# Kernel tuning notes

Hardware: AMD Instinct MI355X
Metric: run time of the kernel (lower is better)

Reference implementation:

```python
import jax, jax.numpy as jnp
import numpy as np

L, H, D, N, M, P, C, IMG, B = 12, 12, 768, 197, 3072, 16, 3, 224, 16
SKIP_AT = (3, 6, 9, 12)


def pos_emb(n, d):
    i = jnp.arange(n, dtype=jnp.float32)[:, None]
    j = jnp.arange(d)[None, :]
    je = (j // 2) * 2  # j for even, j-1 for odd
    ang = i / jnp.power(10000.0, je.astype(jnp.float32) / d)
    return jnp.where(j % 2 == 0, jnp.sin(ang), jnp.cos(ang))  # [n, d]


def layer_norm(x, g, b):
    mu = x.mean(-1, keepdims=True)
    var = x.var(-1, keepdims=True)
    return (x - mu) / jnp.sqrt(var + 1e-5) * g + b


def setup_inputs() -> dict:
    key = jax.random.key(0)
    ks = jax.random.split(key, 16)
    s = 0.02
    f32 = jnp.float32
    return {
        "images": jax.random.normal(ks[0], (B, C, IMG, IMG), f32),
        "class_token": jax.random.uniform(ks[1], (1, D), f32),
        "Wp": jax.random.normal(ks[2], (D, P * P * C), f32) * s,
        "bp": jnp.zeros((D,), f32),
        "Wq": jax.random.normal(ks[3], (L, H, D, D), f32) * s,
        "bq": jnp.zeros((L, H, D), f32),
        "Wk": jax.random.normal(ks[4], (L, H, D, D), f32) * s,
        "bk": jnp.zeros((L, H, D), f32),
        "Wv": jax.random.normal(ks[5], (L, H, D, D), f32) * s,
        "bv": jnp.zeros((L, H, D), f32),
        "Wm": jax.random.normal(ks[6], (L, N, H * N), f32) * s,
        "bm": jnp.zeros((L, N), f32),
        "g1": jnp.ones((L, D), f32),
        "be1": jnp.zeros((L, D), f32),
        "W1": jax.random.normal(ks[7], (L, M, D), f32) * s,
        "b1": jnp.zeros((L, M), f32),
        "W2": jax.random.normal(ks[8], (L, D, M), f32) * s,
        "b2": jnp.zeros((L, D), f32),
        "g2": jnp.ones((L, D), f32),
        "be2": jnp.zeros((L, D), f32),
    }


def reference(images, class_token, Wp, bp, Wq, bq, Wk, bk, Wv, bv, Wm, bm,
              g1, be1, W1, b1, W2, b2, g2, be2):
    b = images.shape[0]
    Hn, Wn = IMG // P, IMG // P
    # einops 'b c (patch_x h) (patch_y w) -> b (h w) (patch_x patch_y c)'
    x = images.reshape(b, C, P, Hn, P, Wn).transpose(0, 3, 5, 2, 4, 1)
    patches = x.reshape(b, Hn * Wn, P * P * C)
    tokens = patches @ Wp.T + bp  # [b, N-1, D]
    cls = jnp.broadcast_to(class_token[None], (b, 1, D))
    out = jnp.concatenate([cls, tokens], axis=1) + pos_emb(N, D)[None]
    scale = 1.0 / jnp.sqrt(jnp.float32(N - 1))
    skips = []
    for l in range(L):
        x0 = out
        q = jnp.einsum('bnd,hed->bhne', x0, Wq[l]) + bq[l][None, :, None, :]
        k = jnp.einsum('bnd,hed->bhne', x0, Wk[l]) + bk[l][None, :, None, :]
        v = jnp.einsum('bnd,hed->bhne', x0, Wv[l]) + bv[l][None, :, None, :]
        attn = jax.nn.softmax(jnp.einsum('bhne,bhme->bhnm', q, k) * scale, axis=-1)
        o = jnp.einsum('bhnm,bhme->bhne', attn, v).reshape(b, H * N, D)
        # transpose -> [b, D, H*N], Linear(H*N -> N), transpose back
        msa = jnp.einsum('bfd,nf->bnd', o, Wm[l]) + bm[l][None, :, None]
        x1 = layer_norm(x0 + msa, g1[l], be1[l])
        hdn = jax.nn.gelu(x1 @ W1[l].T + b1[l], approximate=False)
        out = layer_norm(x1 + (hdn @ W2[l].T + b2[l]), g2[l], be2[l])
        if l + 1 in SKIP_AT:
            skips.append(out[:, 1:, :])
    return (out[:, 1:, :], *skips)
```

## Files before the change

### kernel.cpp

```cpp
#include <hip/hip_runtime.h>
#include <cstdint>
#include <cstddef>

typedef __bf16 bf16;
typedef __bf16 bf16x8 __attribute__((ext_vector_type(8)));
typedef float f32x4 __attribute__((ext_vector_type(4)));

#define DEVINL __device__ __forceinline__

typedef const __attribute__((address_space(1))) void* as1cv;
typedef __attribute__((address_space(3))) void* as3v;

DEVINL void gload16(const bf16* g, bf16* l) {
    __builtin_amdgcn_global_load_lds((as1cv)g, (as3v)l, 16, 0, 0);
}

static constexpr int Lh = 12, Hh = 12, Dh = 768, Nh = 197, Mh = 3072, Bh = 16;
static constexpr int BN   = Bh * Nh;
static constexpr int NPAT = Bh * 196;
static constexpr int HD   = Hh * Dh;
static constexpr int QKN  = 2 * HD;
static constexpr int NP   = 256;
static constexpr int FHN  = Hh * Nh;
static constexpr int FP   = 2368;
static constexpr size_t SEC = (size_t)Bh * 196 * Dh;
static constexpr long LSqk = (long)QKN * Dh;
static constexpr long PART = (long)BN * Dh;

template<int AF32, int BF32, int OUTBF, int BIAS, int ACT, int ZFILL>
__global__ __launch_bounds__(256, 3) void gemm_bt(
    const void* __restrict__ Av, long sAy, long sAz, int lda,
    const void* __restrict__ Bv, long sBy, long sBz, int ldb,
    void* __restrict__ Cv, long sCy, long sCz, int ldc,
    const float* __restrict__ bias, long sBiasY,
    int Mv, int Nv, int K, int tilesN, int kChunk)
{
    __shared__ __align__(16) bf16 Asm[128 * 32];
    __shared__ __align__(16) bf16 Bsm[128 * 32];
    const int bx = blockIdx.x;
    const int tm = bx / tilesN, tn = bx % tilesN;
    const long aoff = (long)blockIdx.y * sAy + (long)blockIdx.z * sAz + (long)tm * 128 * lda;
    const long boff = (long)blockIdx.y * sBy + (long)blockIdx.z * sBz + (long)tn * 128 * ldb;
    const int tid = threadIdx.x;
    const int lane = tid & 63, wid = tid >> 6;
    const int ar = tid >> 2, ac = (tid & 3) << 3;
    const bf16* Ag = (const bf16*)Av + aoff + (long)ar * lda + ac;
    const bf16* Bg = (const bf16*)Bv + boff + (long)ar * ldb + ac;
    const float* Af = (const float*)Av + aoff + (long)ar * lda + ac;
    const float* Bf = (const float*)Bv + boff + (long)ar * ldb + ac;
    bf16* lA = Asm + wid * 512;
    bf16* lB = Bsm + wid * 512;
    const int mw = (wid >> 1) * 64, nw = (wid & 1) * 64;
    const int fr = lane & 15, fq = lane >> 4;
    const int kBeg = kChunk ? blockIdx.y * kChunk : 0;
    const int kEnd = kChunk ? min(K, kBeg + kChunk) : K;
    f32x4 acc[4][4] = {};
    for (int k0 = kBeg; k0 < kEnd; k0 += 32) {
        if (AF32) {
            const float* p0 = Af + k0;
            const float* p1 = p0 + (long)64 * lda;
            f32x4 a0 = *(const f32x4*)p0, a1 = *(const f32x4*)(p0 + 4);
            f32x4 a2 = *(const f32x4*)p1, a3 = *(const f32x4*)(p1 + 4);
            bf16x8 r0, r1;
#pragma unroll
            for (int i = 0; i < 4; i++) { r0[i] = (bf16)a0[i]; r0[i + 4] = (bf16)a1[i];
                                          r1[i] = (bf16)a2[i]; r1[i + 4] = (bf16)a3[i]; }
            *(bf16x8*)&Asm[ar * 32 + ac] = r0;
            *(bf16x8*)&Asm[(ar + 64) * 32 + ac] = r1;
        } else {
            gload16(Ag + k0, lA);
            gload16(Ag + (long)64 * lda + k0, lA + 2048);
        }
        if (BF32) {
            const float* p0 = Bf + k0;
            const float* p1 = p0 + (long)64 * ldb;
            f32x4 a0 = *(const f32x4*)p0, a1 = *(const f32x4*)(p0 + 4);
            f32x4 a2 = *(const f32x4*)p1, a3 = *(const f32x4*)(p1 + 4);
            bf16x8 r0, r1;
#pragma unroll
            for (int i = 0; i < 4; i++) { r0[i] = (bf16)a0[i]; r0[i + 4] = (bf16)a1[i];
                                          r1[i] = (bf16)a2[i]; r1[i + 4] = (bf16)a3[i]; }
            *(bf16x8*)&Bsm[ar * 32 + ac] = r0;
            *(bf16x8*)&Bsm[(ar + 64) * 32 + ac] = r1;
        } else {
            gload16(Bg + k0, lB);
            gload16(Bg + (long)64 * ldb + k0, lB + 2048);
        }
        __syncthreads();
        bf16x8 af[4], bv[4];
#pragma unroll
        for (int i = 0; i < 4; i++) af[i] = *(const bf16x8*)&Asm[(mw + i * 16 + fr) * 32 + (fq << 3)];
#pragma unroll
        for (int j = 0; j < 4; j++) bv[j] = *(const bf16x8*)&Bsm[(nw + j * 16 + fr) * 32 + (fq << 3)];
#pragma unroll
        for (int i = 0; i < 4; i++)
#pragma unroll
            for (int j = 0; j < 4; j++)
                acc[i][j] = __builtin_amdgcn_mfma_f32_16x16x32_bf16(af[i], bv[j], acc[i][j], 0, 0, 0);
        __syncthreads();
    }
    const long cb = (long)blockIdx.y * sCy + (long)blockIdx.z * sCz;
    const float* biasp = bias ? bias + (long)blockIdx.y * sBiasY : nullptr;
#pragma unroll
    for (int i = 0; i < 4; i++) {
        const int row0 = tm * 128 + mw + i * 16 + fq * 4;
#pragma unroll
        for (int j = 0; j < 4; j++) {
            const int col = tn * 128 + nw + j * 16 + fr;
            const bool cok = (col < Nv);
            if (!cok && !ZFILL) continue;
            float bc = (BIAS == 1 && cok) ? biasp[col] : 0.f;
#pragma unroll
            for (int r = 0; r < 4; r++) {
                const int rr = row0 + r;
                if (rr >= Mv) continue;
                float v;
                if (cok) {
                    v = acc[i][j][r];
                    if (BIAS == 1) v += bc;
                    if (BIAS == 2) v += biasp[rr];
                    if (ACT) v = 0.5f * v * (1.f + erff(v * 0.70710678118654752f));
                } else v = 0.f;
                const long ci = cb + (long)rr * ldc + col;
                if (OUTBF) ((bf16*)Cv)[ci] = (bf16)v;
                else       ((float*)Cv)[ci] = v;
            }
        }
    }
}

__global__ __launch_bounds__(512, 2) void qksoft_k(
    const bf16* __restrict__ qkb, bf16* __restrict__ P)
{
    __shared__ __align__(16) bf16 Qs[128 * 32];
    __shared__ __align__(16) bf16 Ks[256 * 32];
    __shared__ float redM[2][64][4];
    __shared__ float redS[2][64][4];
    const int rt = blockIdx.x, h = blockIdx.y, b = blockIdx.z;
    const int tid = threadIdx.x;
    const int lane = tid & 63, wid = tid >> 6;
    const int wr = wid >> 2, wc = wid & 3;
    const int fr = lane & 15, fq = lane >> 4;
    const int ar = tid >> 2, ac = (tid & 3) << 3;
    const bf16* Qg = qkb + ((size_t)b * Nh + rt * 128 + ar) * QKN + h * Dh + ac;
    const bf16* Kg = qkb + ((size_t)b * Nh + ar) * QKN + HD + h * Dh + ac;
    bf16* lQ = Qs + wid * 512;
    bf16* lK = Ks + wid * 512;
    f32x4 acc[4][4] = {};
    for (int k0 = 0; k0 < 768; k0 += 32) {
        gload16(Qg + k0, lQ);
        gload16(Kg + k0, lK);
        gload16(Kg + (size_t)128 * QKN + k0, lK + 4096);
        __syncthreads();
        bf16x8 af[4], bv[4];
#pragma unroll
        for (int i = 0; i < 4; i++) af[i] = *(const bf16x8*)&Qs[(wr * 64 + i * 16 + fr) * 32 + (fq << 3)];
#pragma unroll
        for (int j = 0; j < 4; j++) bv[j] = *(const bf16x8*)&Ks[(wc * 64 + j * 16 + fr) * 32 + (fq << 3)];
#pragma unroll
        for (int i = 0; i < 4; i++)
#pragma unroll
            for (int j = 0; j < 4; j++)
                acc[i][j] = __builtin_amdgcn_mfma_f32_16x16x32_bf16(af[i], bv[j], acc[i][j], 0, 0, 0);
        __syncthreads();
    }
    const float scale = 1.f / 14.f;
    float mx[4][4];
#pragma unroll
    for (int i = 0; i < 4; i++)
#pragma unroll
        for (int r = 0; r < 4; r++) {
            float m0 = -3e30f;
#pragma unroll
            for (int j = 0; j < 4; j++) {
                const int m = wc * 64 + j * 16 + fr;
                float v = (m < Nh) ? acc[i][j][r] * scale : -3e30f;
                acc[i][j][r] = v;
                m0 = fmaxf(m0, v);
            }
            m0 = fmaxf(m0, __shfl_xor(m0, 1));
            m0 = fmaxf(m0, __shfl_xor(m0, 2));
            m0 = fmaxf(m0, __shfl_xor(m0, 4));
            m0 = fmaxf(m0, __shfl_xor(m0, 8));
            mx[i][r] = m0;
        }
    if (fr == 0) {
#pragma unroll
        for (int i = 0; i < 4; i++)
#pragma unroll
            for (int r = 0; r < 4; r++) redM[wr][i * 16 + fq * 4 + r][wc] = mx[i][r];
    }
    __syncthreads();
    float sm[4][4];
#pragma unroll
    for (int i = 0; i < 4; i++)
#pragma unroll
        for (int r = 0; r < 4; r++) {
            const int row = i * 16 + fq * 4 + r;
            const float rm = fmaxf(fmaxf(redM[wr][row][0], redM[wr][row][1]),
                                   fmaxf(redM[wr][row][2], redM[wr][row][3]));
            float s0 = 0.f;
#pragma unroll
            for (int j = 0; j < 4; j++) {
                const float e = expf(acc[i][j][r] - rm);
                acc[i][j][r] = e;
                s0 += e;
            }
            s0 += __shfl_xor(s0, 1);
            s0 += __shfl_xor(s0, 2);
            s0 += __shfl_xor(s0, 4);
            s0 += __shfl_xor(s0, 8);
            sm[i][r] = s0;
        }
    if (fr == 0) {
#pragma unroll
        for (int i = 0; i < 4; i++)
#pragma unroll
            for (int r = 0; r < 4; r++) redS[wr][i * 16 + fq * 4 + r][wc] = sm[i][r];
    }
    __syncthreads();
    bf16* Pb = P + ((size_t)(b * Hh + h) * NP + rt * 128) * NP;
#pragma unroll
    for (int i = 0; i < 4; i++)
#pragma unroll
        for (int r = 0; r < 4; r++) {
            const int row = i * 16 + fq * 4 + r;
            const float s = redS[wr][row][0] + redS[wr][row][1] + redS[wr][row][2] + redS[wr][row][3];
            const float inv = 1.f / s;
#pragma unroll
            for (int j = 0; j < 4; j++)
                Pb[(size_t)(wr * 64 + row) * NP + wc * 64 + j * 16 + fr] = (bf16)(acc[i][j][r] * inv);
        }
}

__global__ __launch_bounds__(256) void cvt_k(const float* __restrict__ in, bf16* __restrict__ out, long n) {
    const long i = ((long)blockIdx.x * 256 + threadIdx.x) * 8;
    if (i >= n) return;
    f32x4 a = *(const f32x4*)(in + i);
    f32x4 b = *(const f32x4*)(in + i + 4);
    bf16x8 r;
#pragma unroll
    for (int j = 0; j < 4; j++) { r[j] = (bf16)a[j]; r[j + 4] = (bf16)b[j]; }
    *(bf16x8*)(out + i) = r;
}

__global__ __launch_bounds__(256) void cvt_s_k(const float* __restrict__ in, bf16* __restrict__ out,
                                               long perLayer, long dstStride, long dstOff, long total) {
    const long i = ((long)blockIdx.x * 256 + threadIdx.x) * 8;
    if (i >= total) return;
    const long l = i / perLayer, r = i % perLayer;
    f32x4 a = *(const f32x4*)(in + i);
    f32x4 b = *(const f32x4*)(in + i + 4);
    bf16x8 v;
#pragma unroll
    for (int j = 0; j < 4; j++) { v[j] = (bf16)a[j]; v[j + 4] = (bf16)b[j]; }
    *(bf16x8*)(out + l * dstStride + dstOff + r) = v;
}

__global__ void qkbias_k(const float* __restrict__ bq, const float* __restrict__ bk, float* __restrict__ dst) {
    const int idx = blockIdx.x * 256 + threadIdx.x;
    if (idx >= Lh * QKN) return;
    const int l = idx / QKN, c = idx % QKN;
    dst[idx] = (c < HD) ? bq[l * HD + c] : bk[l * HD + c - HD];
}

__global__ void patch_k(const float* __restrict__ images, bf16* __restrict__ patches) {
    const long idx = (long)blockIdx.x * 256 + threadIdx.x;
    if (idx >= (long)NPAT * Dh) return;
    const int r = (int)(idx / Dh), f = (int)(idx % Dh);
    const int b = r / 196, pi = r % 196, h = pi / 14, w = pi % 14;
    const int px = f / 48, rem = f % 48, py = rem / 3, c = rem % 3;
    patches[idx] = (bf16)images[(((long)(b * 3 + c) * 224) + px * 14 + h) * 224 + py * 14 + w];
}

__global__ void assemble_k(const float* __restrict__ tokens, const float* __restrict__ cls,
                           float* __restrict__ x, bf16* __restrict__ xbf) {
    const long idx = (long)blockIdx.x * 256 + threadIdx.x;
    if (idx >= (long)BN * Dh) return;
    const int r = (int)(idx / Dh), d = (int)(idx % Dh);
    const int b = r / Nh, n = r % Nh;
    const int je = d & ~1;
    const float ang = (float)n / powf(10000.f, (float)je / 768.f);
    const float pe = (d & 1) ? cosf(ang) : sinf(ang);
    const float val = (n == 0) ? (cls[d] + pe)
                               : (tokens[((long)b * 196 + (n - 1)) * Dh + d] + pe);
    x[idx] = val;
    xbf[idx] = (bf16)val;
}

__global__ void wmpad_k(const float* __restrict__ Wm, bf16* __restrict__ WmP) {
    const long idx = (long)blockIdx.x * 256 + threadIdx.x;
    if (idx >= (long)Lh * 256 * FP) return;
    const int l = (int)(idx / (256 * FP));
    const int rem = (int)(idx % (256 * FP));
    const int n = rem / FP, f = rem % FP;
    bf16 v = (bf16)0.f;
    if (n < Nh && f < FHN) v = (bf16)Wm[((long)l * Nh + n) * FHN + f];
    WmP[idx] = v;
}

__global__ void otpad_k(bf16* __restrict__ oT, int cb) {
    const int idx = blockIdx.x * 256 + threadIdx.x;
    if (idx >= cb * Dh * 4) return;
    const int b = idx / (Dh * 4), rem = idx % (Dh * 4), e = rem / 4, f = rem % 4;
    oT[((long)b * Dh + e) * FP + FHN + f] = (bf16)0.f;
}

__global__ __launch_bounds__(256) void softmax_k(const float* __restrict__ S, bf16* __restrict__ P) {
    const int tid = threadIdx.x, lane = tid & 63, wv = tid >> 6;
    const long rr = (long)blockIdx.x * 4 + wv;
    const int bh = (int)(rr / Nh), n = (int)(rr % Nh);
    const float* s = S + ((long)bh * Nh + n) * NP;
    bf16* p = P + ((long)bh * NP + n) * NP;
    float v[4]; float mx = -1e30f;
#pragma unroll
    for (int i = 0; i < 4; i++) {
        const int c = lane + i * 64;
        const float t = (c < Nh) ? s[c] * (1.f / 14.f) : -1e30f;
        v[i] = t; mx = fmaxf(mx, t);
    }
    for (int o = 32; o; o >>= 1) mx = fmaxf(mx, __shfl_xor(mx, o));
    float sum = 0.f;
#pragma unroll
    for (int i = 0; i < 4; i++) {
        const int c = lane + i * 64;
        v[i] = (c < Nh) ? expf(v[i] - mx) : 0.f;
        sum += v[i];
    }
    for (int o = 32; o; o >>= 1) sum += __shfl_xor(sum, o);
    const float inv = 1.f / sum;
#pragma unroll
    for (int i = 0; i < 4; i++) p[lane + i * 64] = (bf16)(v[i] * inv);
}

template<int BIAS_ROW, int NPART>
__global__ __launch_bounds__(256) void add_ln_k(
    const float* __restrict__ in1, const float* __restrict__ in2, long pstride,
    const float* __restrict__ bias, const float* __restrict__ gamma, const float* __restrict__ beta,
    float* __restrict__ outF, bf16* __restrict__ outBF,
    float* __restrict__ dst0, float* __restrict__ dst1)
{
    const int r = blockIdx.x;
    const int b = r / Nh, n = r % Nh;
    const long base = (long)r * Dh;
    const int tid = threadIdx.x;
    const float rowb = BIAS_ROW ? bias[n] : 0.f;
    float v[3]; float s = 0.f, s2 = 0.f;
#pragma unroll
    for (int i = 0; i < 3; i++) {
        const int d = tid + 256 * i;
        float t = in1[base + d] + (BIAS_ROW ? rowb : bias[d]);
#pragma unroll
        for (int pp = 0; pp < NPART; pp++) t += in2[pp * pstride + base + d];
        v[i] = t; s += t; s2 += t * t;
    }
    for (int o = 32; o; o >>= 1) { s += __shfl_xor(s, o); s2 += __shfl_xor(s2, o); }
    __shared__ float red[8];
    const int lane = tid & 63, wv = tid >> 6;
    if (lane == 0) { red[wv] = s; red[4 + wv] = s2; }
    __syncthreads();
    s  = red[0] + red[1] + red[2] + red[3];
    s2 = red[4] + red[5] + red[6] + red[7];
    const float mu = s * (1.f / 768.f);
    const float var = s2 * (1.f / 768.f) - mu * mu;
    const float rs = rsqrtf(var + 1e-5f);
    const long ob = ((long)b * 196 + (n - 1)) * Dh;
#pragma unroll
    for (int i = 0; i < 3; i++) {
        const int d = tid + 256 * i;
        const float y = (v[i] - mu) * rs * gamma[d] + beta[d];
        outF[base + d] = y;
        outBF[base + d] = (bf16)y;
        if (n > 0) {
            if (dst0) dst0[ob + d] = y;
            if (dst1) dst1[ob + d] = y;
        }
    }
}

static inline size_t al256(size_t x) { return (x + 255) & ~(size_t)255; }

extern "C" void kernel_launch(void* const* d_in, const int* in_sizes, int n_in,
                              void* d_out, int out_size, void* d_ws, size_t ws_size,
                              hipStream_t stream) {
    (void)in_sizes; (void)n_in; (void)out_size;
    const float* images = (const float*)d_in[0];
    const float* cls    = (const float*)d_in[1];
    const float* Wp     = (const float*)d_in[2];
    const float* bp     = (const float*)d_in[3];
    const float* Wq     = (const float*)d_in[4];
    const float* bq     = (const float*)d_in[5];
    const float* Wk     = (const float*)d_in[6];
    const float* bk     = (const float*)d_in[7];
    const float* Wv     = (const float*)d_in[8];
    const float* bv     = (const float*)d_in[9];
    const float* Wm     = (const float*)d_in[10];
    const float* bm     = (const float*)d_in[11];
    const float* g1     = (const float*)d_in[12];
    const float* be1    = (const float*)d_in[13];
    const float* W1     = (const float*)d_in[14];
    const float* b1     = (const float*)d_in[15];
    const float* W2     = (const float*)d_in[16];
    const float* b2     = (const float*)d_in[17];
    const float* g2     = (const float*)d_in[18];
    const float* be2    = (const float*)d_in[19];
    float* out = (float*)d_out;

    const size_t xB    = al256(3152ull * 768 * 4);
    const size_t xbfB  = al256(3328ull * 768 * 2);
    const size_t x1B   = al256(3152ull * 768 * 4);
    const size_t x1bfB = al256(3200ull * 768 * 2);
    const size_t msaB  = al256(4ull * PART * 4);
    const size_t mlp2B = al256(4ull * PART * 4);
    const size_t wmpB  = al256(12ull * 256 * FP * 2);
    const size_t qkbB  = al256((size_t)Lh * QKN * 4);
    const size_t persistB = xB + xbfB + x1B + x1bfB + msaB + mlp2B + wmpB + qkbB;
    const size_t hdnB  = al256(3200ull * 3072 * 2);
    const size_t preB  = al256(3200ull * 768 * 2) + al256(3136ull * 768 * 4);
    const size_t wqkvB = al256((size_t)Lh * HD * Dh * 2);
    const size_t w12B  = al256((size_t)Lh * Mh * Dh * 2);
    const size_t wpB   = al256(768ull * 768 * 2);
    const size_t weightsB = 3 * wqkvB + 2 * w12B + wpB;

    auto chunk_bytes = [&](int cb, size_t& qbB_o, size_t& vtB_o, size_t& sB_o) -> size_t {
        const size_t qbRows = (size_t)((cb * 197 + 127) / 128 + 1) * 128;
        size_t qbB = al256(qbRows * HD * 2);
        size_t vtB = al256((size_t)cb * Hh * Dh * NP * 2);
        size_t sB  = al256((size_t)cb * Hh * Nh * NP * 4);
        size_t c = 2 * qbB + vtB + sB;
        if (c < hdnB) c = hdnB;
        if (c < preB) c = preB;
        qbB_o = qbB; vtB_o = vtB; sB_o = sB;
        return c;
    };
    const size_t margin = (size_t)(8u << 20);
    const size_t pBf  = al256((size_t)Bh * Hh * NP * NP * 2);
    const size_t otBf = al256((size_t)Bh * Dh * FP * 2);
    size_t qbBf, vtBf, sBf;
    size_t chunkF = chunk_bytes(16, qbBf, vtBf, sBf) + pBf + otBf;
    bool fused = (chunkF + persistB + weightsB + margin <= ws_size);

    int CB = 16; bool useCvt = true;
    size_t qbB, vtB, sB, chunkB;
    if (fused) {
        chunkB = chunkF; qbB = qbBf; vtB = vtBf; sB = sBf;
    } else {
        for (;;) {
            chunkB = chunk_bytes(CB, qbB, vtB, sB);
            if (chunkB + persistB + weightsB + margin <= ws_size) break;
            if (CB == 1) { useCvt = false; break; }
            CB >>= 1;
        }
        if (!useCvt) {
            CB = 16;
            for (;;) {
                chunkB = chunk_bytes(CB, qbB, vtB, sB);
                if (chunkB + persistB + margin <= ws_size || CB == 1) break;
                CB >>= 1;
            }
        }
    }

    char* wsb = (char*)d_ws;
    bf16*  qb  = (bf16*)wsb;
    bf16*  kb  = (bf16*)(wsb + qbB);
    bf16*  vT  = (bf16*)(wsb + 2 * qbB);
    float* S   = (float*)(wsb + 2 * qbB + vtB);
    bf16*  P2  = (bf16*)(wsb + 2 * qbB + vtB + sB);
    bf16*  oT2 = (bf16*)(wsb + 2 * qbB + vtB + sB + pBf);
    bf16*  oT  = fused ? oT2 : qb;
    bf16*  P   = fused ? P2  : kb;
    bf16*  hdn = (bf16*)wsb;
    bf16*  patches = (bf16*)wsb;
    float* tokens  = (float*)(wsb + al256(3200ull * 768 * 2));
    char* p = wsb + chunkB;
    float* x    = (float*)p; p += xB;
    bf16*  xbf  = (bf16*) p; p += xbfB;
    float* x1   = (float*)p; p += x1B;
    bf16*  x1bf = (bf16*) p; p += x1bfB;
    float* msaP = (float*)p; p += msaB;
    float* mlp2P= (float*)p; p += mlp2B;
    bf16*  WmP  = (bf16*) p; p += wmpB;
    float* qkbiasF = (float*)p; p += qkbB;
    bf16 *WqkB = nullptr, *WvB = nullptr, *W1B = nullptr, *W2B = nullptr, *WpB = nullptr;
    const bool cvt = fused || useCvt;
    if (cvt) {
        WqkB = (bf16*)p; p += 2 * wqkvB;
        WvB  = (bf16*)p; p += wqkvB;
        W1B  = (bf16*)p; p += w12B;
        W2B  = (bf16*)p; p += w12B;
        WpB  = (bf16*)p; p += wpB;
    }

    if (cvt) {
        const long nqkv = (long)Lh * HD * Dh;
        const long n12  = (long)Lh * Mh * Dh;
        const int gq = (int)((nqkv / 8 + 255) / 256);
        const int g12 = (int)((n12 / 8 + 255) / 256);
        cvt_s_k<<<gq, 256, 0, stream>>>(Wq, WqkB, (long)HD * Dh, LSqk, 0, nqkv);
        cvt_s_k<<<gq, 256, 0, stream>>>(Wk, WqkB, (long)HD * Dh, LSqk, (long)HD * Dh, nqkv);
        cvt_k<<<gq, 256, 0, stream>>>(Wv, WvB, nqkv);
        cvt_k<<<g12, 256, 0, stream>>>(W1, W1B, n12);
        cvt_k<<<g12, 256, 0, stream>>>(W2, W2B, n12);
        cvt_k<<<(768 * 768 / 8 + 255) / 256, 256, 0, stream>>>(Wp, WpB, 768 * 768);
        qkbias_k<<<(Lh * QKN + 255) / 256, 256, 0, stream>>>(bq, bk, qkbiasF);
    }

    patch_k<<<9408, 256, 0, stream>>>(images, patches);
    if (cvt)
        gemm_bt<0, 0, 0, 1, 0, 0><<<dim3(25 * 6), 256, 0, stream>>>(
            patches, 0, 0, 768, WpB, 0, 0, 768, tokens, 0, 0, 768, bp, 0, NPAT, 768, 768, 6, 0);
    else
        gemm_bt<0, 1, 0, 1, 0, 0><<<dim3(25 * 6), 256, 0, stream>>>(
            patches, 0, 0, 768, Wp, 0, 0, 768, tokens, 0, 0, 768, bp, 0, NPAT, 768, 768, 6, 0);
    assemble_k<<<9456, 256, 0, stream>>>(tokens, cls, x, xbf);
    wmpad_k<<<28416, 256, 0, stream>>>(Wm, WmP);
    if (fused) otpad_k<<<16 * 12, 256, 0, stream>>>(oT2, 16);

    const int NCH = 16 / CB;
    const int tilesQ = (CB * 197 + 127) / 128;

    for (int l = 0; l < 12; l++) {
        const float* Wq_l = Wq + (size_t)l * HD * Dh;
        const float* Wk_l = Wk + (size_t)l * HD * Dh;
        const float* Wv_l = Wv + (size_t)l * HD * Dh;
        const bf16* WqkB_l = cvt ? WqkB + (size_t)l * LSqk : nullptr;
        const bf16* WqB_l = WqkB_l;
        const bf16* WkB_l = cvt ? WqkB_l + (size_t)HD * Dh : nullptr;
        const bf16* WvB_l = cvt ? WvB + (size_t)l * HD * Dh : nullptr;
        const float* bq_l = bq + (size_t)l * HD;
        const float* bk_l = bk + (size_t)l * HD;
        const float* bv_l = bv + (size_t)l * HD;
        const bf16*  WmP_l = WmP + (size_t)l * 256 * FP;
        const float* bm_l = bm + (size_t)l * Nh;
        const float* g1_l = g1 + (size_t)l * Dh;  const float* be1_l = be1 + (size_t)l * Dh;
        const float* W1_l = W1 + (size_t)l * Mh * Dh; const float* b1_l = b1 + (size_t)l * Mh;
        const float* W2_l = W2 + (size_t)l * Dh * Mh; const float* b2_l = b2 + (size_t)l * Dh;
        const bf16* W1B_l = cvt ? W1B + (size_t)l * Mh * Dh : nullptr;
        const bf16* W2B_l = cvt ? W2B + (size_t)l * Mh * Dh : nullptr;
        const float* g2_l = g2 + (size_t)l * Dh;  const float* be2_l = be2 + (size_t)l * Dh;

        if (fused) {
            gemm_bt<0, 0, 1, 1, 0, 0><<<dim3(25 * 144), 256, 0, stream>>>(
                xbf, 0, 0, 768, WqkB_l, 0, 0, 768, qb, 0, 0, QKN,
                qkbiasF + (size_t)l * QKN, 0, BN, QKN, 768, 144, 0);
            gemm_bt<0, 0, 1, 2, 0, 1><<<dim3(12, 12, 16), 256, 0, stream>>>(
                WvB_l, (long)Dh * Dh, 0, 768,
                xbf, 0, (long)Nh * Dh, 768,
                vT, (long)Dh * NP, (long)Hh * Dh * NP, NP,
                bv_l, Dh, 768, Nh, 768, 2, 0);
            qksoft_k<<<dim3(2, Hh, Bh), 512, 0, stream>>>(qb, P);
            gemm_bt<0, 0, 1, 0, 0, 0><<<dim3(12, 12, 16), 256, 0, stream>>>(
                vT, (long)Dh * NP, (long)Hh * Dh * NP, NP,
                P, (long)NP * NP, (long)Hh * NP * NP, NP,
                oT, (long)Nh, (long)Dh * FP, FP,
                nullptr, 0, Dh, Nh, NP, 2, 0);
            gemm_bt<0, 0, 0, 0, 0, 0><<<dim3(12, 4, 16), 256, 0, stream>>>(
                WmP_l, 0, 0, FP,
                oT, 0, (long)Dh * FP, FP,
                msaP, PART, (long)Nh * Dh, Dh,
                nullptr, 0, Nh, Dh, FP, 6, 608);
        } else {
            for (int c = 0; c < NCH; c++) {
                const size_t r0 = (size_t)c * CB * Nh;
                if (useCvt) {
                    gemm_bt<0, 0, 1, 1, 0, 0><<<dim3(tilesQ * 72), 256, 0, stream>>>(
                        xbf + r0 * Dh, 0, 0, 768, WqB_l, 0, 0, 768, qb, 0, 0, HD, bq_l, 0, CB * Nh, HD, 768, 72, 0);
                    gemm_bt<0, 0, 1, 1, 0, 0><<<dim3(tilesQ * 72), 256, 0, stream>>>(
                        xbf + r0 * Dh, 0, 0, 768, WkB_l, 0, 0, 768, kb, 0, 0, HD, bk_l, 0, CB * Nh, HD, 768, 72, 0);
                    gemm_bt<0, 0, 1, 2, 0, 1><<<dim3(12, 12, CB), 256, 0, stream>>>(
                        WvB_l, (long)Dh * Dh, 0, 768,
                        xbf + r0 * Dh, 0, (long)Nh * Dh, 768,
                        vT, (long)Dh * NP, (long)Hh * Dh * NP, NP,
                        bv_l, Dh, 768, Nh, 768, 2, 0);
                } else {
                    gemm_bt<0, 1, 1, 1, 0, 0><<<dim3(tilesQ * 72), 256, 0, stream>>>(
                        xbf + r0 * Dh, 0, 0, 768, Wq_l, 0, 0, 768, qb, 0, 0, HD, bq_l, 0, CB * Nh, HD, 768, 72, 0);
                    gemm_bt<0, 1, 1, 1, 0, 0><<<dim3(tilesQ * 72), 256, 0, stream>>>(
                        xbf + r0 * Dh, 0, 0, 768, Wk_l, 0, 0, 768, kb, 0, 0, HD, bk_l, 0, CB * Nh, HD, 768, 72, 0);
                    gemm_bt<1, 0, 1, 2, 0, 1><<<dim3(12, 12, CB), 256, 0, stream>>>(
                        Wv_l, (long)Dh * Dh, 0, 768,
                        xbf + r0 * Dh, 0, (long)Nh * Dh, 768,
                        vT, (long)Dh * NP, (long)Hh * Dh * NP, NP,
                        bv_l, Dh, 768, Nh, 768, 2, 0);
                }
                gemm_bt<0, 0, 0, 0, 0, 0><<<dim3(4, 12, CB), 256, 0, stream>>>(
                    qb, Dh, (long)Nh * HD, HD,
                    kb, Dh, (long)Nh * HD, HD,
                    S, (long)Nh * NP, (long)Hh * Nh * NP, NP,
                    nullptr, 0, Nh, Nh, 768, 2, 0);
                softmax_k<<<CB * 591, 256, 0, stream>>>(S, P);
                otpad_k<<<CB * 12, 256, 0, stream>>>(oT, CB);
                gemm_bt<0, 0, 1, 0, 0, 0><<<dim3(12, 12, CB), 256, 0, stream>>>(
                    vT, (long)Dh * NP, (long)Hh * Dh * NP, NP,
                    P, (long)NP * NP, (long)Hh * NP * NP, NP,
                    oT, (long)Nh, (long)Dh * FP, FP,
                    nullptr, 0, Dh, Nh, NP, 2, 0);
                gemm_bt<0, 0, 0, 0, 0, 0><<<dim3(12, 4, CB), 256, 0, stream>>>(
                    WmP_l, 0, 0, FP,
                    oT, 0, (long)Dh * FP, FP,
                    msaP + r0 * Dh, PART, (long)Nh * Dh, Dh,
                    nullptr, 0, Nh, Dh, FP, 6, 608);
            }
        }
        add_ln_k<1, 4><<<BN, 256, 0, stream>>>(x, msaP, PART, bm_l, g1_l, be1_l, x1, x1bf, nullptr, nullptr);
        if (cvt) {
            gemm_bt<0, 0, 1, 1, 1, 0><<<dim3(25 * 24), 256, 0, stream>>>(
                x1bf, 0, 0, 768, W1B_l, 0, 0, 768, hdn, 0, 0, Mh, b1_l, 0, BN, Mh, 768, 24, 0);
            gemm_bt<0, 0, 0, 0, 0, 0><<<dim3(25 * 6, 4, 1), 256, 0, stream>>>(
                hdn, 0, 0, Mh, W2B_l, 0, 0, Mh, mlp2P, PART, 0, Dh, nullptr, 0, BN, Dh, Mh, 6, 768);
        } else {
            gemm_bt<0, 1, 1, 1, 1, 0><<<dim3(25 * 24), 256, 0, stream>>>(
                x1bf, 0, 0, 768, W1_l, 0, 0, 768, hdn, 0, 0, Mh, b1_l, 0, BN, Mh, 768, 24, 0);
            gemm_bt<0, 1, 0, 0, 0, 0><<<dim3(25 * 6, 4, 1), 256, 0, stream>>>(
                hdn, 0, 0, Mh, W2_l, 0, 0, Mh, mlp2P, PART, 0, Dh, nullptr, 0, BN, Dh, Mh, 6, 768);
        }
        float* d0 = nullptr; float* d1 = nullptr;
        if (l == 2)  d0 = out + 1 * SEC;
        if (l == 5)  d0 = out + 2 * SEC;
        if (l == 8)  d0 = out + 3 * SEC;
        if (l == 11) { d0 = out; d1 = out + 4 * SEC; }
        add_ln_k<0, 4><<<BN, 256, 0, stream>>>(x1, mlp2P, PART, b2_l, g2_l, be2_l, x, xbf, d0, d1);
    }
}
```

Baseline: 6.228 ms.

## Fuse V projection into single QKV GEMM and transpose V separately

Concatenates the bf16 Q, K and V weights and their biases so that one GEMM produces Q, K and V in a single row-major buffer. The separate batched, zero-filled V-transposed GEMM is replaced by a small LDS tile-transpose kernel that writes V into the padded vT layout. The fused GEMM gets a larger grid and better occupancy, and X is read once instead of twice, in exchange for an extra transpose pass over V and a larger intermediate buffer. The workspace sizing for the fused path is recomputed to match.

```diff
diff --git a/kernel.cpp b/kernel.cpp
--- a/kernel.cpp
+++ b/kernel.cpp
@@ -20,11 +20,12 @@
 static constexpr int NPAT = Bh * 196;
 static constexpr int HD   = Hh * Dh;
 static constexpr int QKN  = 2 * HD;
+static constexpr int QKV3 = 3 * HD;
 static constexpr int NP   = 256;
 static constexpr int FHN  = Hh * Nh;
 static constexpr int FP   = 2368;
 static constexpr size_t SEC = (size_t)Bh * 196 * Dh;
-static constexpr long LSqk = (long)QKN * Dh;
+static constexpr long LS3 = (long)QKV3 * Dh;
 static constexpr long PART = (long)BN * Dh;
 
 template<int AF32, int BF32, int OUTBF, int BIAS, int ACT, int ZFILL>
@@ -142,15 +143,15 @@
     const int wr = wid >> 2, wc = wid & 3;
     const int fr = lane & 15, fq = lane >> 4;
     const int ar = tid >> 2, ac = (tid & 3) << 3;
-    const bf16* Qg = qkb + ((size_t)b * Nh + rt * 128 + ar) * QKN + h * Dh + ac;
-    const bf16* Kg = qkb + ((size_t)b * Nh + ar) * QKN + HD + h * Dh + ac;
+    const bf16* Qg = qkb + ((size_t)b * Nh + rt * 128 + ar) * QKV3 + h * Dh + ac;
+    const bf16* Kg = qkb + ((size_t)b * Nh + ar) * QKV3 + HD + h * Dh + ac;
     bf16* lQ = Qs + wid * 512;
     bf16* lK = Ks + wid * 512;
     f32x4 acc[4][4] = {};
     for (int k0 = 0; k0 < 768; k0 += 32) {
         gload16(Qg + k0, lQ);
         gload16(Kg + k0, lK);
-        gload16(Kg + (size_t)128 * QKN + k0, lK + 4096);
+        gload16(Kg + (size_t)128 * QKV3 + k0, lK + 4096);
         __syncthreads();
         bf16x8 af[4], bv[4];
 #pragma unroll
@@ -233,6 +234,31 @@
         }
 }
 
+__global__ __launch_bounds__(256) void vtrans_k(const bf16* __restrict__ qkv, bf16* __restrict__ vT) {
+    __shared__ bf16 t[64][72];
+    const int eb = (blockIdx.x >> 2) << 6;
+    const int nb = (blockIdx.x & 3) << 6;
+    const int h = blockIdx.y, b = blockIdx.z;
+    const int tid = threadIdx.x;
+    const int lr = tid >> 2;
+    const int lc = (tid & 3) << 4;
+    const int n = nb + lr;
+    if (n < Nh) {
+        const bf16* src = qkv + (size_t)(b * Nh + n) * QKV3 + 2 * HD + h * Dh + eb + lc;
+        *(bf16x8*)&t[lr][lc] = *(const bf16x8*)src;
+        *(bf16x8*)&t[lr][lc + 8] = *(const bf16x8*)(src + 8);
+    } else {
+        bf16x8 z = {};
+        *(bf16x8*)&t[lr][lc] = z; *(bf16x8*)&t[lr][lc + 8] = z;
+    }
+    __syncthreads();
+    bf16* dst = vT + ((size_t)(b * Hh + h) * Dh + eb + lr) * NP + nb + lc;
+    bf16x8 o0, o1;
+#pragma unroll
+    for (int j = 0; j < 8; j++) { o0[j] = t[lc + j][lr]; o1[j] = t[lc + 8 + j][lr]; }
+    *(bf16x8*)dst = o0; *(bf16x8*)(dst + 8) = o1;
+}
+
 __global__ __launch_bounds__(256) void cvt_k(const float* __restrict__ in, bf16* __restrict__ out, long n) {
     const long i = ((long)blockIdx.x * 256 + threadIdx.x) * 8;
     if (i >= n) return;
@@ -257,11 +283,16 @@
     *(bf16x8*)(out + l * dstStride + dstOff + r) = v;
 }
 
-__global__ void qkbias_k(const float* __restrict__ bq, const float* __restrict__ bk, float* __restrict__ dst) {
+__global__ void qkvbias_k(const float* __restrict__ bq, const float* __restrict__ bk,
+                          const float* __restrict__ bv, float* __restrict__ dst) {
     const int idx = blockIdx.x * 256 + threadIdx.x;
-    if (idx >= Lh * QKN) return;
-    const int l = idx / QKN, c = idx % QKN;
-    dst[idx] = (c < HD) ? bq[l * HD + c] : bk[l * HD + c - HD];
+    if (idx >= Lh * QKV3) return;
+    const int l = idx / QKV3, c = idx % QKV3;
+    float v;
+    if (c < HD) v = bq[l * HD + c];
+    else if (c < 2 * HD) v = bk[l * HD + c - HD];
+    else v = bv[l * HD + c - 2 * HD];
+    dst[idx] = v;
 }
 
 __global__ void patch_k(const float* __restrict__ images, bf16* __restrict__ patches) {
@@ -413,14 +444,24 @@
     const size_t msaB  = al256(4ull * PART * 4);
     const size_t mlp2B = al256(4ull * PART * 4);
     const size_t wmpB  = al256(12ull * 256 * FP * 2);
-    const size_t qkbB  = al256((size_t)Lh * QKN * 4);
-    const size_t persistB = xB + xbfB + x1B + x1bfB + msaB + mlp2B + wmpB + qkbB;
+    const size_t biasB = al256((size_t)Lh * QKV3 * 4);
+    const size_t persistB = xB + xbfB + x1B + x1bfB + msaB + mlp2B + wmpB + biasB;
     const size_t hdnB  = al256(3200ull * 3072 * 2);
     const size_t preB  = al256(3200ull * 768 * 2) + al256(3136ull * 768 * 4);
     const size_t wqkvB = al256((size_t)Lh * HD * Dh * 2);
     const size_t w12B  = al256((size_t)Lh * Mh * Dh * 2);
     const size_t wpB   = al256(768ull * 768 * 2);
     const size_t weightsB = 3 * wqkvB + 2 * w12B + wpB;
+
+    const size_t qkvbB = al256(3328ull * QKV3 * 2);
+    const size_t vtBf  = al256((size_t)Bh * Hh * Dh * NP * 2);
+    const size_t pBf   = al256((size_t)Bh * Hh * NP * NP * 2);
+    const size_t otBf  = al256((size_t)Bh * Dh * FP * 2);
+    size_t chunkF = qkvbB + vtBf + pBf + otBf;
+    if (chunkF < hdnB) chunkF = hdnB;
+    if (chunkF < preB) chunkF = preB;
+    const size_t margin = (size_t)(8u << 20);
+    const bool fused = (chunkF + persistB + weightsB + margin <= ws_size);
 
     auto chunk_bytes = [&](int cb, size_t& qbB_o, size_t& vtB_o, size_t& sB_o) -> size_t {
         const size_t qbRows = (size_t)((cb * 197 + 127) / 128 + 1) * 128;
@@ -433,17 +474,10 @@
         qbB_o = qbB; vtB_o = vtB; sB_o = sB;
         return c;
     };
-    const size_t margin = (size_t)(8u << 20);
-    const size_t pBf  = al256((size_t)Bh * Hh * NP * NP * 2);
-    const size_t otBf = al256((size_t)Bh * Dh * FP * 2);
-    size_t qbBf, vtBf, sBf;
-    size_t chunkF = chunk_bytes(16, qbBf, vtBf, sBf) + pBf + otBf;
-    bool fused = (chunkF + persistB + weightsB + margin <= ws_size);
-
     int CB = 16; bool useCvt = true;
     size_t qbB, vtB, sB, chunkB;
     if (fused) {
-        chunkB = chunkF; qbB = qbBf; vtB = vtBf; sB = sBf;
+        chunkB = chunkF; qbB = vtB = sB = 0;
     } else {
         for (;;) {
             chunkB = chunk_bytes(CB, qbB, vtB, sB);
@@ -462,12 +496,15 @@
     }
 
     char* wsb = (char*)d_ws;
+    bf16*  qkvb = (bf16*)wsb;
+    bf16*  vT2  = (bf16*)(wsb + qkvbB);
+    bf16*  P2   = (bf16*)(wsb + qkvbB + vtBf);
+    bf16*  oT2  = (bf16*)(wsb + qkvbB + vtBf + pBf);
     bf16*  qb  = (bf16*)wsb;
     bf16*  kb  = (bf16*)(wsb + qbB);
-    bf16*  vT  = (bf16*)(wsb + 2 * qbB);
+    bf16*  vTf = (bf16*)(wsb + 2 * qbB);
     float* S   = (float*)(wsb + 2 * qbB + vtB);
-    bf16*  P2  = (bf16*)(wsb + 2 * qbB + vtB + sB);
-    bf16*  oT2 = (bf16*)(wsb + 2 * qbB + vtB + sB + pBf);
+    bf16*  vT  = fused ? vT2 : vTf;
     bf16*  oT  = fused ? oT2 : qb;
     bf16*  P   = fused ? P2  : kb;
     bf16*  hdn = (bf16*)wsb;
@@ -481,12 +518,11 @@
     float* msaP = (float*)p; p += msaB;
     float* mlp2P= (float*)p; p += mlp2B;
     bf16*  WmP  = (bf16*) p; p += wmpB;
-    float* qkbiasF = (float*)p; p += qkbB;
-    bf16 *WqkB = nullptr, *WvB = nullptr, *W1B = nullptr, *W2B = nullptr, *WpB = nullptr;
+    float* qkvbias = (float*)p; p += biasB;
+    bf16 *WqkvB = nullptr, *W1B = nullptr, *W2B = nullptr, *WpB = nullptr;
     const bool cvt = fused || useCvt;
     if (cvt) {
-        WqkB = (bf16*)p; p += 2 * wqkvB;
-        WvB  = (bf16*)p; p += wqkvB;
+        WqkvB = (bf16*)p; p += 3 * wqkvB;
         W1B  = (bf16*)p; p += w12B;
         W2B  = (bf16*)p; p += w12B;
         WpB  = (bf16*)p; p += wpB;
@@ -497,13 +533,13 @@
         const long n12  = (long)Lh * Mh * Dh;
         const int gq = (int)((nqkv / 8 + 255) / 256);
         const int g12 = (int)((n12 / 8 + 255) / 256);
-        cvt_s_k<<<gq, 256, 0, stream>>>(Wq, WqkB, (long)HD * Dh, LSqk, 0, nqkv);
-        cvt_s_k<<<gq, 256, 0, stream>>>(Wk, WqkB, (long)HD * Dh, LSqk, (long)HD * Dh, nqkv);
-        cvt_k<<<gq, 256, 0, stream>>>(Wv, WvB, nqkv);
+        cvt_s_k<<<gq, 256, 0, stream>>>(Wq, WqkvB, (long)HD * Dh, LS3, 0, nqkv);
+        cvt_s_k<<<gq, 256, 0, stream>>>(Wk, WqkvB, (long)HD * Dh, LS3, (long)HD * Dh, nqkv);
+        cvt_s_k<<<gq, 256, 0, stream>>>(Wv, WqkvB, (long)HD * Dh, LS3, 2L * HD * Dh, nqkv);
         cvt_k<<<g12, 256, 0, stream>>>(W1, W1B, n12);
         cvt_k<<<g12, 256, 0, stream>>>(W2, W2B, n12);
         cvt_k<<<(768 * 768 / 8 + 255) / 256, 256, 0, stream>>>(Wp, WpB, 768 * 768);
-        qkbias_k<<<(Lh * QKN + 255) / 256, 256, 0, stream>>>(bq, bk, qkbiasF);
+        qkvbias_k<<<(Lh * QKV3 + 255) / 256, 256, 0, stream>>>(bq, bk, bv, qkvbias);
     }
 
     patch_k<<<9408, 256, 0, stream>>>(images, patches);
@@ -524,10 +560,10 @@
         const float* Wq_l = Wq + (size_t)l * HD * Dh;
         const float* Wk_l = Wk + (size_t)l * HD * Dh;
         const float* Wv_l = Wv + (size_t)l * HD * Dh;
-        const bf16* WqkB_l = cvt ? WqkB + (size_t)l * LSqk : nullptr;
-        const bf16* WqB_l = WqkB_l;
-        const bf16* WkB_l = cvt ? WqkB_l + (size_t)HD * Dh : nullptr;
-        const bf16* WvB_l = cvt ? WvB + (size_t)l * HD * Dh : nullptr;
+        const bf16* Wqkv_l = cvt ? WqkvB + (size_t)l * LS3 : nullptr;
+        const bf16* WqB_l = Wqkv_l;
+        const bf16* WkB_l = cvt ? Wqkv_l + (size_t)HD * Dh : nullptr;
+        const bf16* WvB_l = cvt ? Wqkv_l + 2 * (size_t)HD * Dh : nullptr;
         const float* bq_l = bq + (size_t)l * HD;
         const float* bk_l = bk + (size_t)l * HD;
         const float* bv_l = bv + (size_t)l * HD;
@@ -541,15 +577,11 @@
         const float* g2_l = g2 + (size_t)l * Dh;  const float* be2_l = be2 + (size_t)l * Dh;
 
         if (fused) {
-            gemm_bt<0, 0, 1, 1, 0, 0><<<dim3(25 * 144), 256, 0, stream>>>(
-                xbf, 0, 0, 768, WqkB_l, 0, 0, 768, qb, 0, 0, QKN,
-                qkbiasF + (size_t)l * QKN, 0, BN, QKN, 768, 144, 0);
-            gemm_bt<0, 0, 1, 2, 0, 1><<<dim3(12, 12, 16), 256, 0, stream>>>(
-                WvB_l, (long)Dh * Dh, 0, 768,
-                xbf, 0, (long)Nh * Dh, 768,
-                vT, (long)Dh * NP, (long)Hh * Dh * NP, NP,
-                bv_l, Dh, 768, Nh, 768, 2, 0);
-            qksoft_k<<<dim3(2, Hh, Bh), 512, 0, stream>>>(qb, P);
+            gemm_bt<0, 0, 1, 1, 0, 0><<<dim3(25 * 216), 256, 0, stream>>>(
+                xbf, 0, 0, 768, Wqkv_l, 0, 0, 768, qkvb, 0, 0, QKV3,
+                qkvbias + (size_t)l * QKV3, 0, BN, QKV3, 768, 216, 0);
+            vtrans_k<<<dim3(48, 12, 16), 256, 0, stream>>>(qkvb, vT);
+            qksoft_k<<<dim3(2, Hh, Bh), 512, 0, stream>>>(qkvb, P);
             gemm_bt<0, 0, 1, 0, 0, 0><<<dim3(12, 12, 16), 256, 0, stream>>>(
                 vT, (long)Dh * NP, (long)Hh * Dh * NP, NP,
                 P, (long)NP * NP, (long)Hh * NP * NP, NP,
```

Result: no change. 6.219 ms (-0.1%).
